# Kernel tuning notes

Hardware: AMD Instinct MI355X
Metric: run time of the kernel (lower is better)

Reference implementation:

```python
import jax, jax.numpy as jnp
import numpy as np

N = 524288   # total graph nodes
V = 64       # number of virtual nodes (clusters)
C = N // V   # nodes per cluster (8192)
D = 256      # in_feats
H = 256      # hidden_feats
EPS = 1e-5


def setup_inputs() -> dict:
    key = jax.random.key(0)
    ks = jax.random.split(key, 8)
    sD = 1.0 / np.sqrt(D)
    sH = 1.0 / np.sqrt(2 * H)
    inp = {
        "x": jax.random.normal(ks[0], (N, D), dtype=jnp.float32),
        "vn_emb": jax.random.normal(ks[1], (V, D), dtype=jnp.float32) * 0.1,
        "wq": jax.random.normal(ks[2], (D, D), dtype=jnp.float32) * sD,
        "wk": jax.random.normal(ks[3], (D, D), dtype=jnp.float32) * sD,
        "v_attn": jax.random.normal(ks[4], (D,), dtype=jnp.float32) * sD,
        "w1": jax.random.normal(ks[5], (D, 2 * H), dtype=jnp.float32) * sD,
        "b1": jnp.zeros((2 * H,), dtype=jnp.float32),
        "g1": jnp.ones((2 * H,), dtype=jnp.float32),
        "beta1": jnp.zeros((2 * H,), dtype=jnp.float32),
        "w2": jax.random.normal(ks[6], (2 * H, H), dtype=jnp.float32) * sH,
        "b2": jnp.zeros((H,), dtype=jnp.float32),
        "g2": jnp.ones((H,), dtype=jnp.float32),
        "beta2": jnp.zeros((H,), dtype=jnp.float32),
        # cluster v owns contiguous node block [v*C, (v+1)*C)
        "vn_index": jnp.arange(N, dtype=jnp.int32).reshape(V, C),
        "vn_indices": jnp.stack(
            [jnp.arange(N, dtype=jnp.int32), (jnp.arange(N, dtype=jnp.int32) // C)],
            axis=1),
    }
    return inp


def _batchnorm(z, g, b):
    # training-mode BN over the virtual-node batch dim
    m = jnp.mean(z, axis=0)
    v = jnp.var(z, axis=0)
    return (z - m) * jax.lax.rsqrt(v + EPS) * g + b


def reference(x, vn_emb, wq, wk, v_attn, w1, b1, g1, beta1,
              w2, b2, g2, beta2, vn_index, vn_indices):
    vx = vn_emb                                   # [V, D]
    # --- update_node_emb (layer 0): broadcast-add VN emb to its nodes ---
    h = x + vx[vn_indices[:, 1]]                  # [N, D]
    # --- update_vn_emb: per-cluster additive attention pooling (vectorized over V) ---
    cluster_h = h[vn_index]                       # [V, C, D]
    q = vx @ wq                                   # [V, D]
    kproj = jnp.einsum('vcd,de->vce', cluster_h, wk)   # [V, C, D]
    scores = jnp.einsum('vce,e->vc', jnp.tanh(kproj + q[:, None, :]), v_attn)
    attn = jax.nn.softmax(scores, axis=-1)        # [V, C]
    pooled = jnp.einsum('vc,vcd->vd', attn, cluster_h) + vx  # [V, D]
    # --- mlp_vns[0]: Linear -> BN -> ReLU -> Linear -> BN -> ReLU ---
    z = jax.nn.relu(_batchnorm(pooled @ w1 + b1, g1, beta1))  # [V, 2H]
    vx_new = jax.nn.relu(_batchnorm(z @ w2 + b2, g2, beta2))  # [V, H]
    return h, vx_new
```

## Files before the change

kernel.cpp:

```cpp
#include <hip/hip_runtime.h>


typedef __bf16 bf16x8 __attribute__((ext_vector_type(8)));
typedef float f32x4 __attribute__((ext_vector_type(4)));
typedef unsigned short us8 __attribute__((ext_vector_type(8)));

__device__ __forceinline__ unsigned short f2bf(float f) {
  unsigned int u = __float_as_uint(f);
  return (unsigned short)((u + 0x7fffu + ((u >> 16) & 1u)) >> 16);
}
__device__ __forceinline__ float tanh_fast(float x) {
  float cx = fminf(fmaxf(x, -15.f), 15.f);
  float e = __expf(2.f * cx);
  return (e - 1.f) * __builtin_amdgcn_rcpf(e + 1.f);
}
__device__ __forceinline__ float wave_sum(float v) {
#pragma unroll
  for (int o = 1; o < 64; o <<= 1) v += __shfl_xor(v, o);
  return v;
}
__device__ __forceinline__ void lgkm_barrier() {
  asm volatile("s_waitcnt lgkmcnt(0)" ::: "memory");
  __builtin_amdgcn_sched_barrier(0);
  __builtin_amdgcn_s_barrier();
  __builtin_amdgcn_sched_barrier(0);
}
__device__ __forceinline__ void gll16(const float* gp, float* lp) {
  __builtin_amdgcn_global_load_lds(
      (const __attribute__((address_space(1))) void*)gp,
      (__attribute__((address_space(3))) void*)lp, 16, 0, 0);
}

__global__ __launch_bounds__(256) void k_prep(
    const float* __restrict__ vn_emb, const float* __restrict__ wq,
    const float* __restrict__ wk, float* __restrict__ qg,
    unsigned short* __restrict__ wkp) {
  int t = threadIdx.x;
  int b = blockIdx.x;
  if (b < 64) {
    float a = 0.f;
#pragma unroll 4
    for (int d = 0; d < 256; ++d) a += vn_emb[(b << 8) + d] * wq[(d << 8) + t];
    qg[(b << 8) + t] = a;
  } else {
    int tid = ((b - 64) << 8) + t;
    int l = tid & 63;
    int ks = (tid >> 6) & 7;
    int ct = tid >> 9;
    int col = (ct << 4) + (l & 15);
    int d0 = (ks << 5) + ((l >> 4) << 3);
    us8 o;
#pragma unroll
    for (int e = 0; e < 8; ++e) o[e] = f2bf(wk[(d0 + e) * 256 + col]);
    *reinterpret_cast<us8*>(wkp + (size_t)tid * 8) = o;
  }
}

__global__ __launch_bounds__(512, 2) void k_main(
    const float* __restrict__ x, const float* __restrict__ vn_emb,
    const float* __restrict__ v_attn, const float* __restrict__ qg,
    const unsigned short* __restrict__ wkp, float* __restrict__ hout,
    float* __restrict__ vecs, float* __restrict__ Zb) {
  __shared__ float stage[2][32 * 256];
  __shared__ unsigned short hs[32 * 256];
  __shared__ float vxs[256], qv[256], va[256];
  __shared__ float spbuf[8][32];

  const int t = threadIdx.x;
  const int blk = blockIdx.x;
  const int cl = blk >> 2;

  if (t < 256) {
    vxs[t] = vn_emb[(cl << 8) + t];
    qv[t] = qg[(cl << 8) + t];
    va[t] = v_attn[t];
  }

  const int l = t & 63, wv = t >> 6;
  const int lr = l & 15, lg = l >> 4;
  const int rg = wv & 1, ctq = wv >> 1;

  bf16x8 wkf[4][8];
#pragma unroll
  for (int c = 0; c < 4; ++c)
#pragma unroll
    for (int ks = 0; ks < 8; ++ks) {
      const int ct = (ctq << 2) + c;
      wkf[c][ks] = __builtin_bit_cast(
          bf16x8, *reinterpret_cast<const us8*>(
                      wkp + ((size_t)((((ct << 3) + ks) << 6) + l)) * 8));
    }

  char* hsb = reinterpret_cast<char*>(hs);
  const size_t growbase = ((size_t)blk << 11) + (wv << 2);
  const int srow0 = wv << 2;

  f32x4 acc = {0.f, 0.f, 0.f, 0.f};
  float zacc = 0.f;

#pragma unroll
  for (int tt = 0; tt < 2; ++tt)
#pragma unroll
    for (int i = 0; i < 4; ++i)
      gll16(x + (((growbase + (tt << 5) + i) << 8) + (l << 2)),
            &stage[tt][(srow0 + i) << 8]);

  __syncthreads();

  const f32x4 vv = *reinterpret_cast<const f32x4*>(&vxs[l << 2]);
  f32x4 hh0, hh1, hh2, hh3;

  for (int tile = 0; tile < 64; ++tile) {
    if (tile == 63) {
      asm volatile("s_waitcnt vmcnt(0)" ::: "memory");
    } else {
      asm volatile("s_waitcnt vmcnt(4)" ::: "memory");
    }
    __builtin_amdgcn_sched_barrier(0);

    const float* sb = &stage[tile & 1][0];
    const size_t hg0 = ((growbase + ((size_t)tile << 5)) << 8) + (l << 2);
#define S1(hhX, i)                                                          \
  {                                                                         \
    f32x4 sv = *reinterpret_cast<const f32x4*>(                             \
        &sb[((srow0 + i) << 8) + (l << 2)]);                                \
    hhX = sv + vv;                                                          \
    *reinterpret_cast<f32x4*>(hout + hg0 + ((size_t)i << 8)) = hhX;         \
    ushort4 o;                                                              \
    o.x = f2bf(hhX[0]);                                                     \
    o.y = f2bf(hhX[1]);                                                     \
    o.z = f2bf(hhX[2]);                                                     \
    o.w = f2bf(hhX[3]);                                                     \
    int row = srow0 + i;                                                    \
    *reinterpret_cast<ushort4*>(                                            \
        hsb + ((row << 9) + ((l << 3) ^ ((row & 7) << 4)))) = o;            \
  }
    S1(hh0, 0) S1(hh1, 1) S1(hh2, 2) S1(hh3, 3)
#undef S1

    __builtin_amdgcn_sched_barrier(0);
    if (tile < 62) {
      const int tt = tile + 2;
#pragma unroll
      for (int i = 0; i < 4; ++i)
        gll16(x + (((growbase + ((size_t)tt << 5) + i) << 8) + (l << 2)),
              &stage[tile & 1][(srow0 + i) << 8]);
    }
    lgkm_barrier();

    bf16x8 bfr[8];
    {
      int row2 = (rg << 4) + lr;
      int sw = (row2 & 7) << 4;
#pragma unroll
      for (int ks = 0; ks < 8; ++ks)
        bfr[ks] = __builtin_bit_cast(
            bf16x8, *reinterpret_cast<const us8*>(
                        hsb + ((row2 << 9) + ((((ks << 6) + (lg << 4))) ^ sw))));
    }
    float sp = 0.f;
#pragma unroll
    for (int c = 0; c < 4; ++c) {
      const int ct = (ctq << 2) + c;
      f32x4 ac0 = {0.f, 0.f, 0.f, 0.f};
#pragma unroll
      for (int ks = 0; ks < 8; ++ks)
        ac0 = __builtin_amdgcn_mfma_f32_16x16x32_bf16(wkf[c][ks], bfr[ks], ac0,
                                                      0, 0, 0);
      const int eo0 = (ct << 4) + (lg << 2);
      const f32x4 qf = *reinterpret_cast<const f32x4*>(&qv[eo0]);
      const f32x4 vf = *reinterpret_cast<const f32x4*>(&va[eo0]);
#pragma unroll
      for (int r = 0; r < 4; ++r) sp += tanh_fast(ac0[r] + qf[r]) * vf[r];
    }
    sp += __shfl_xor(sp, 16);
    sp += __shfl_xor(sp, 32);
    if (lg == 0) spbuf[(ctq << 1) | rg][lr | (rg << 4)] = sp;
    lgkm_barrier();

    float srow = 0.f;
    if (l < 32) {
      int rh = l >> 4;
#pragma unroll
      for (int q = 0; q < 4; ++q) srow += spbuf[(q << 1) | rh][l];
    }
    float w_all = __expf(srow);
    if (wv == 0 && l < 32) zacc += w_all;
    {
      float wn0 = __shfl(w_all, srow0 + 0);
      float wn1 = __shfl(w_all, srow0 + 1);
      float wn2 = __shfl(w_all, srow0 + 2);
      float wn3 = __shfl(w_all, srow0 + 3);
      acc += wn0 * hh0 + wn1 * hh1 + wn2 * hh2 + wn3 * hh3;
    }
  }

  __syncthreads();
  float* sc = reinterpret_cast<float*>(hs);
  *reinterpret_cast<f32x4*>(&sc[(wv << 8) + (l << 2)]) = acc;
  __syncthreads();
  if (t < 256) {
    float s = 0.f;
#pragma unroll
    for (int w8 = 0; w8 < 8; ++w8) s += sc[(w8 << 8) + t];
    vecs[((size_t)blk << 8) + t] = s;
  }
  if (wv == 0) {
    float z = wave_sum(zacc);
    if (l == 0) Zb[blk] = z;
  }
}

__global__ __launch_bounds__(256) void k_combine(
    const float* __restrict__ vecs, const float* __restrict__ Zb,
    const float* __restrict__ vn_emb, float* __restrict__ pooledT) {
  int v = blockIdx.x, t = threadIdx.x;
  float s = 0.f, z = 0.f;
#pragma unroll
  for (int b = 0; b < 4; ++b) {
    s += vecs[(size_t)(((v << 2) + b) << 8) + t];
    z += Zb[(v << 2) + b];
  }
  pooledT[(t << 6) + v] = s / z + vn_emb[(v << 8) + t];
}

__global__ __launch_bounds__(64) void k_mlp1(
    const float* __restrict__ pooledT, const float* __restrict__ w1,
    const float* __restrict__ b1, const float* __restrict__ g1,
    const float* __restrict__ be1, float* __restrict__ z1T) {
  int j = blockIdx.x, v = threadIdx.x;
  float a = 0.f;
#pragma unroll 4
  for (int d = 0; d < 256; ++d) a += pooledT[(d << 6) + v] * w1[(d << 9) + j];
  a += b1[j];
  float mu = wave_sum(a) * (1.f / 64.f);
  float df = a - mu;
  float var = wave_sum(df * df) * (1.f / 64.f);
  float z = df * rsqrtf(var + 1e-5f) * g1[j] + be1[j];
  z1T[(j << 6) + v] = fmaxf(z, 0.f);
}

__global__ __launch_bounds__(64) void k_mlp2(
    const float* __restrict__ z1T, const float* __restrict__ w2,
    const float* __restrict__ b2, const float* __restrict__ g2,
    const float* __restrict__ be2, float* __restrict__ vout) {
  int j = blockIdx.x, v = threadIdx.x;
  float a = 0.f;
#pragma unroll 4
  for (int k = 0; k < 512; ++k) a += z1T[(k << 6) + v] * w2[(k << 8) + j];
  a += b2[j];
  float mu = wave_sum(a) * (1.f / 64.f);
  float df = a - mu;
  float var = wave_sum(df * df) * (1.f / 64.f);
  float z = df * rsqrtf(var + 1e-5f) * g2[j] + be2[j];
  vout[(v << 8) + j] = fmaxf(z, 0.f);
}

extern "C" void kernel_launch(void* const* d_in, const int* in_sizes, int n_in,
                              void* d_out, int out_size, void* d_ws,
                              size_t ws_size, hipStream_t stream) {
  const float* x = (const float*)d_in[0];
  const float* vn_emb = (const float*)d_in[1];
  const float* wq = (const float*)d_in[2];
  const float* wk = (const float*)d_in[3];
  const float* v_attn = (const float*)d_in[4];
  const float* w1 = (const float*)d_in[5];
  const float* b1 = (const float*)d_in[6];
  const float* g1 = (const float*)d_in[7];
  const float* beta1 = (const float*)d_in[8];
  const float* w2 = (const float*)d_in[9];
  const float* b2 = (const float*)d_in[10];
  const float* g2 = (const float*)d_in[11];
  const float* beta2 = (const float*)d_in[12];

  char* wsb = (char*)d_ws;
  float* qg = (float*)(wsb + 0);
  unsigned short* wkp = (unsigned short*)(wsb + 65536);
  float* vecs = (float*)(wsb + 196608);
  float* Zb = (float*)(wsb + 458752);
  float* pooledT = (float*)(wsb + 462848);
  float* z1T = (float*)(wsb + 528384);

  float* hout = (float*)d_out;
  float* vout = hout + (size_t)524288 * 256;

  k_prep<<<96, 256, 0, stream>>>(vn_emb, wq, wk, qg, wkp);
  k_main<<<256, 512, 0, stream>>>(x, vn_emb, v_attn, qg, wkp, hout, vecs, Zb);
  k_combine<<<64, 256, 0, stream>>>(vecs, Zb, vn_emb, pooledT);
  k_mlp1<<<512, 64, 0, stream>>>(pooledT, w1, b1, g1, beta1, z1T);
  k_mlp2<<<256, 64, 0, stream>>>(z1T, w2, b2, g2, beta2, vout);
}
```

Before: 325.8 us.

## Split fused main kernel into streaming h-write pass and separate bf16 pooling pass

Replaces the single fused kernel (256 blocks, which computes h, stages it in LDS and does the MFMA attention pooling) with two kernels when the workspace is large enough. A simple streaming kernel writes h and a bf16 copy of h to workspace. A second 1024-block kernel reads the bf16 copy and computes the attention scores and weighted pooling. The goal is more parallelism and simpler bandwidth-bound streaming, at the cost of an extra 256MB write and read of the bf16 intermediate. Pooling also now accumulates from bf16-rounded h rather than fp32.

```diff
diff --git a/kernel.cpp b/kernel.cpp
--- a/kernel.cpp
+++ b/kernel.cpp
@@ -8,6 +8,9 @@
 __device__ __forceinline__ unsigned short f2bf(float f) {
   unsigned int u = __float_as_uint(f);
   return (unsigned short)((u + 0x7fffu + ((u >> 16) & 1u)) >> 16);
+}
+__device__ __forceinline__ float bf2f(unsigned short s) {
+  return __uint_as_float(((unsigned int)s) << 16);
 }
 __device__ __forceinline__ float tanh_fast(float x) {
   float cx = fminf(fmaxf(x, -15.f), 15.f);
@@ -56,6 +59,122 @@
   }
 }
 
+__global__ __launch_bounds__(256) void k_stream(
+    const float* __restrict__ x, const float* __restrict__ vn_emb,
+    float* __restrict__ hout, ushort4* __restrict__ hbf4) {
+  const int t = threadIdx.x, blk = blockIdx.x;
+  const int cl = blk >> 6;
+  const size_t base = ((size_t)blk << 13);
+  const f32x4 vv = *reinterpret_cast<const f32x4*>(
+      &vn_emb[(cl << 8) + ((t & 63) << 2)]);
+  const f32x4* xv = reinterpret_cast<const f32x4*>(x);
+  f32x4* hv = reinterpret_cast<f32x4*>(hout);
+#pragma unroll 8
+  for (int i = 0; i < 32; ++i) {
+    const size_t id = base + (i << 8) + t;
+    f32x4 h = xv[id] + vv;
+    hv[id] = h;
+    ushort4 o;
+    o.x = f2bf(h[0]);
+    o.y = f2bf(h[1]);
+    o.z = f2bf(h[2]);
+    o.w = f2bf(h[3]);
+    hbf4[id] = o;
+  }
+}
+
+__global__ __launch_bounds__(256, 3) void k_pool(
+    const ushort4* __restrict__ hbf4, const float* __restrict__ v_attn,
+    const float* __restrict__ qg, const unsigned short* __restrict__ wkp,
+    float* __restrict__ vecs, float* __restrict__ Zb) {
+  __shared__ unsigned short hs[4][16 * 256];
+  __shared__ float qv[256], va[256];
+  __shared__ float zr[4];
+
+  const int t = threadIdx.x;
+  const int blk = blockIdx.x;
+  const int cl = blk >> 4;
+
+  qv[t] = qg[(cl << 8) + t];
+  va[t] = v_attn[t];
+  __syncthreads();
+
+  const int l = t & 63, wv = t >> 6;
+  const int lr = l & 15, lg = l >> 4;
+
+  char* myhs = reinterpret_cast<char*>(hs[wv]);
+  f32x4 acc = {0.f, 0.f, 0.f, 0.f};
+  float zacc = 0.f;
+
+  const size_t wrow0 = ((size_t)blk << 9) + ((size_t)wv << 7);
+
+  for (int chunk = 0; chunk < 8; ++chunk) {
+    const size_t row0 = wrow0 + ((size_t)chunk << 4);
+
+#pragma unroll
+    for (int i = 0; i < 16; ++i) {
+      ushort4 hv4 = hbf4[((row0 + i) << 6) + l];
+      *reinterpret_cast<ushort4*>(
+          myhs + ((i << 9) + ((l << 3) ^ ((i & 7) << 4)))) = hv4;
+    }
+    asm volatile("s_waitcnt lgkmcnt(0)" ::: "memory");
+    __builtin_amdgcn_sched_barrier(0);
+
+    bf16x8 bfr[8];
+    {
+      const int sw = (lr & 7) << 4;
+#pragma unroll
+      for (int ks = 0; ks < 8; ++ks)
+        bfr[ks] = __builtin_bit_cast(
+            bf16x8, *reinterpret_cast<const us8*>(
+                        myhs + ((lr << 9) + ((((ks << 6) + (lg << 4))) ^ sw))));
+    }
+
+    float sp = 0.f;
+#pragma unroll 4
+    for (int ct = 0; ct < 16; ++ct) {
+      f32x4 ac0 = {0.f, 0.f, 0.f, 0.f};
+#pragma unroll
+      for (int ks = 0; ks < 8; ++ks) {
+        bf16x8 af = __builtin_bit_cast(
+            bf16x8, *reinterpret_cast<const us8*>(
+                        wkp + ((size_t)((((ct << 3) + ks) << 6) + l)) * 8));
+        ac0 = __builtin_amdgcn_mfma_f32_16x16x32_bf16(af, bfr[ks], ac0, 0, 0, 0);
+      }
+      const int eo0 = (ct << 4) + (lg << 2);
+      const f32x4 qf = *reinterpret_cast<const f32x4*>(&qv[eo0]);
+      const f32x4 vf = *reinterpret_cast<const f32x4*>(&va[eo0]);
+#pragma unroll
+      for (int r = 0; r < 4; ++r) sp += tanh_fast(ac0[r] + qf[r]) * vf[r];
+    }
+    sp += __shfl_xor(sp, 16);
+    sp += __shfl_xor(sp, 32);
+    float w = __expf(sp);
+    zacc += w;
+
+#pragma unroll
+    for (int n = 0; n < 16; ++n) {
+      float wn = __shfl(w, n);
+      ushort4 hv4 = *reinterpret_cast<const ushort4*>(
+          myhs + ((n << 9) + ((l << 3) ^ ((n & 7) << 4))));
+      acc[0] += wn * bf2f(hv4.x);
+      acc[1] += wn * bf2f(hv4.y);
+      acc[2] += wn * bf2f(hv4.z);
+      acc[3] += wn * bf2f(hv4.w);
+    }
+  }
+
+  __syncthreads();
+  float* sc = reinterpret_cast<float*>(hs);
+  *reinterpret_cast<f32x4*>(&sc[(wv << 8) + (l << 2)]) = acc;
+  float zsum = wave_sum(zacc) * 0.25f;
+  if (l == 0) zr[wv] = zsum;
+  __syncthreads();
+  vecs[((size_t)blk << 8) + t] =
+      sc[t] + sc[256 + t] + sc[512 + t] + sc[768 + t];
+  if (t == 0) Zb[blk] = zr[0] + zr[1] + zr[2] + zr[3];
+}
+
 __global__ __launch_bounds__(512, 2) void k_main(
     const float* __restrict__ x, const float* __restrict__ vn_emb,
     const float* __restrict__ v_attn, const float* __restrict__ qg,
@@ -213,13 +332,12 @@
 
 __global__ __launch_bounds__(256) void k_combine(
     const float* __restrict__ vecs, const float* __restrict__ Zb,
-    const float* __restrict__ vn_emb, float* __restrict__ pooledT) {
+    const float* __restrict__ vn_emb, float* __restrict__ pooledT, int nb) {
   int v = blockIdx.x, t = threadIdx.x;
   float s = 0.f, z = 0.f;
-#pragma unroll
-  for (int b = 0; b < 4; ++b) {
-    s += vecs[(size_t)(((v << 2) + b) << 8) + t];
-    z += Zb[(v << 2) + b];
+  for (int b = 0; b < nb; ++b) {
+    s += vecs[((size_t)(v * nb + b) << 8) + t];
+    z += Zb[v * nb + b];
   }
   pooledT[(t << 6) + v] = s / z + vn_emb[(v << 8) + t];
 }
@@ -277,16 +395,27 @@
   float* qg = (float*)(wsb + 0);
   unsigned short* wkp = (unsigned short*)(wsb + 65536);
   float* vecs = (float*)(wsb + 196608);
-  float* Zb = (float*)(wsb + 458752);
-  float* pooledT = (float*)(wsb + 462848);
-  float* z1T = (float*)(wsb + 528384);
+  float* Zb = (float*)(wsb + 1245184);
+  float* pooledT = (float*)(wsb + 1253376);
+  float* z1T = (float*)(wsb + 1318912);
+  ushort4* hbf4 = (ushort4*)(wsb + 2097152);
+
+  const size_t need_big = 2097152 + (size_t)524288 * 256 * 2;
+  const bool big = ws_size >= need_big;
 
   float* hout = (float*)d_out;
   float* vout = hout + (size_t)524288 * 256;
 
   k_prep<<<96, 256, 0, stream>>>(vn_emb, wq, wk, qg, wkp);
-  k_main<<<256, 512, 0, stream>>>(x, vn_emb, v_attn, qg, wkp, hout, vecs, Zb);
-  k_combine<<<64, 256, 0, stream>>>(vecs, Zb, vn_emb, pooledT);
+  if (big) {
+    k_stream<<<4096, 256, 0, stream>>>(x, vn_emb, hout, hbf4);
+    k_pool<<<1024, 256, 0, stream>>>(hbf4, v_attn, qg, wkp, vecs, Zb);
+    k_combine<<<64, 256, 0, stream>>>(vecs, Zb, vn_emb, pooledT, 16);
+  } else {
+    k_main<<<256, 512, 0, stream>>>(x, vn_emb, v_attn, qg, wkp, hout, vecs,
+                                    Zb);
+    k_combine<<<64, 256, 0, stream>>>(vecs, Zb, vn_emb, pooledT, 4);
+  }
   k_mlp1<<<512, 64, 0, stream>>>(pooledT, w1, b1, g1, beta1, z1T);
   k_mlp2<<<256, 64, 0, stream>>>(z1T, w2, b2, g2, beta2, vout);
 }
```

Result: slower. 649.1 us (+99.2%).

## Double wave count in main kernel to 16 waves per 1024-thread block

Applied to the files above, without the earlier changes.

Reworks the main attention-pooling kernel to run 16 waves per block instead of 8. Each wave now owns one 16-column output tile of the key projection and streams two rows per tile instead of four. Each wave also holds a quarter of the previous weight-fragment registers and hoists the q/v_attn loads out of the loop. The aim is more waves in flight per CU to hide memory latency on this streaming kernel. The cost is more barrier participants, a larger score-reduction buffer and fewer outstanding loads per wave.

```diff
diff --git a/kernel.cpp b/kernel.cpp
--- a/kernel.cpp
+++ b/kernel.cpp
@@ -56,7 +56,7 @@
   }
 }
 
-__global__ __launch_bounds__(512, 2) void k_main(
+__global__ __launch_bounds__(1024) void k_main16(
     const float* __restrict__ x, const float* __restrict__ vn_emb,
     const float* __restrict__ v_attn, const float* __restrict__ qg,
     const unsigned short* __restrict__ wkp, float* __restrict__ hout,
@@ -64,7 +64,7 @@
   __shared__ float stage[2][32 * 256];
   __shared__ unsigned short hs[32 * 256];
   __shared__ float vxs[256], qv[256], va[256];
-  __shared__ float spbuf[8][32];
+  __shared__ float spbuf[16][32];
 
   const int t = threadIdx.x;
   const int blk = blockIdx.x;
@@ -78,22 +78,18 @@
 
   const int l = t & 63, wv = t >> 6;
   const int lr = l & 15, lg = l >> 4;
-  const int rg = wv & 1, ctq = wv >> 1;
-
-  bf16x8 wkf[4][8];
-#pragma unroll
-  for (int c = 0; c < 4; ++c)
-#pragma unroll
-    for (int ks = 0; ks < 8; ++ks) {
-      const int ct = (ctq << 2) + c;
-      wkf[c][ks] = __builtin_bit_cast(
-          bf16x8, *reinterpret_cast<const us8*>(
-                      wkp + ((size_t)((((ct << 3) + ks) << 6) + l)) * 8));
-    }
+  const int ct = wv;
+  const int srow0 = wv << 1;
+
+  bf16x8 wkf[8];
+#pragma unroll
+  for (int ks = 0; ks < 8; ++ks)
+    wkf[ks] = __builtin_bit_cast(
+        bf16x8, *reinterpret_cast<const us8*>(
+                    wkp + ((size_t)((((ct << 3) + ks) << 6) + l)) * 8));
 
   char* hsb = reinterpret_cast<char*>(hs);
-  const size_t growbase = ((size_t)blk << 11) + (wv << 2);
-  const int srow0 = wv << 2;
+  const size_t growbase = ((size_t)blk << 11) + srow0;
 
   f32x4 acc = {0.f, 0.f, 0.f, 0.f};
   float zacc = 0.f;
@@ -101,20 +97,23 @@
 #pragma unroll
   for (int tt = 0; tt < 2; ++tt)
 #pragma unroll
-    for (int i = 0; i < 4; ++i)
+    for (int i = 0; i < 2; ++i)
       gll16(x + (((growbase + (tt << 5) + i) << 8) + (l << 2)),
             &stage[tt][(srow0 + i) << 8]);
 
   __syncthreads();
 
   const f32x4 vv = *reinterpret_cast<const f32x4*>(&vxs[l << 2]);
-  f32x4 hh0, hh1, hh2, hh3;
+  const int eo0 = (ct << 4) + (lg << 2);
+  const f32x4 qf = *reinterpret_cast<const f32x4*>(&qv[eo0]);
+  const f32x4 vf = *reinterpret_cast<const f32x4*>(&va[eo0]);
+  f32x4 hh0, hh1;
 
   for (int tile = 0; tile < 64; ++tile) {
     if (tile == 63) {
       asm volatile("s_waitcnt vmcnt(0)" ::: "memory");
     } else {
-      asm volatile("s_waitcnt vmcnt(4)" ::: "memory");
+      asm volatile("s_waitcnt vmcnt(2)" ::: "memory");
     }
     __builtin_amdgcn_sched_barrier(0);
 
@@ -135,63 +134,57 @@
     *reinterpret_cast<ushort4*>(                                            \
         hsb + ((row << 9) + ((l << 3) ^ ((row & 7) << 4)))) = o;            \
   }
-    S1(hh0, 0) S1(hh1, 1) S1(hh2, 2) S1(hh3, 3)
+    S1(hh0, 0) S1(hh1, 1)
 #undef S1
 
     __builtin_amdgcn_sched_barrier(0);
     if (tile < 62) {
       const int tt = tile + 2;
 #pragma unroll
-      for (int i = 0; i < 4; ++i)
+      for (int i = 0; i < 2; ++i)
         gll16(x + (((growbase + ((size_t)tt << 5) + i) << 8) + (l << 2)),
               &stage[tile & 1][(srow0 + i) << 8]);
     }
     lgkm_barrier();
 
-    bf16x8 bfr[8];
-    {
-      int row2 = (rg << 4) + lr;
-      int sw = (row2 & 7) << 4;
+#pragma unroll
+    for (int rg = 0; rg < 2; ++rg) {
+      bf16x8 bfr[8];
+      {
+        int row2 = (rg << 4) + lr;
+        int sw = (row2 & 7) << 4;
+#pragma unroll
+        for (int ks = 0; ks < 8; ++ks)
+          bfr[ks] = __builtin_bit_cast(
+              bf16x8,
+              *reinterpret_cast<const us8*>(
+                  hsb + ((row2 << 9) + ((((ks << 6) + (lg << 4))) ^ sw))));
+      }
+      f32x4 ac0 = {0.f, 0.f, 0.f, 0.f};
 #pragma unroll
       for (int ks = 0; ks < 8; ++ks)
-        bfr[ks] = __builtin_bit_cast(
-            bf16x8, *reinterpret_cast<const us8*>(
-                        hsb + ((row2 << 9) + ((((ks << 6) + (lg << 4))) ^ sw))));
-    }
-    float sp = 0.f;
-#pragma unroll
-    for (int c = 0; c < 4; ++c) {
-      const int ct = (ctq << 2) + c;
-      f32x4 ac0 = {0.f, 0.f, 0.f, 0.f};
-#pragma unroll
-      for (int ks = 0; ks < 8; ++ks)
-        ac0 = __builtin_amdgcn_mfma_f32_16x16x32_bf16(wkf[c][ks], bfr[ks], ac0,
-                                                      0, 0, 0);
-      const int eo0 = (ct << 4) + (lg << 2);
-      const f32x4 qf = *reinterpret_cast<const f32x4*>(&qv[eo0]);
-      const f32x4 vf = *reinterpret_cast<const f32x4*>(&va[eo0]);
+        ac0 = __builtin_amdgcn_mfma_f32_16x16x32_bf16(wkf[ks], bfr[ks], ac0, 0,
+                                                      0, 0);
+      float sp = 0.f;
 #pragma unroll
       for (int r = 0; r < 4; ++r) sp += tanh_fast(ac0[r] + qf[r]) * vf[r];
-    }
-    sp += __shfl_xor(sp, 16);
-    sp += __shfl_xor(sp, 32);
-    if (lg == 0) spbuf[(ctq << 1) | rg][lr | (rg << 4)] = sp;
+      sp += __shfl_xor(sp, 16);
+      sp += __shfl_xor(sp, 32);
+      if (lg == 0) spbuf[ct][(rg << 4) + lr] = sp;
+    }
     lgkm_barrier();
 
     float srow = 0.f;
     if (l < 32) {
-      int rh = l >> 4;
-#pragma unroll
-      for (int q = 0; q < 4; ++q) srow += spbuf[(q << 1) | rh][l];
+#pragma unroll
+      for (int q = 0; q < 16; ++q) srow += spbuf[q][l];
     }
     float w_all = __expf(srow);
     if (wv == 0 && l < 32) zacc += w_all;
     {
       float wn0 = __shfl(w_all, srow0 + 0);
       float wn1 = __shfl(w_all, srow0 + 1);
-      float wn2 = __shfl(w_all, srow0 + 2);
-      float wn3 = __shfl(w_all, srow0 + 3);
-      acc += wn0 * hh0 + wn1 * hh1 + wn2 * hh2 + wn3 * hh3;
+      acc += wn0 * hh0 + wn1 * hh1;
     }
   }
 
@@ -202,7 +195,7 @@
   if (t < 256) {
     float s = 0.f;
 #pragma unroll
-    for (int w8 = 0; w8 < 8; ++w8) s += sc[(w8 << 8) + t];
+    for (int w16 = 0; w16 < 16; ++w16) s += sc[(w16 << 8) + t];
     vecs[((size_t)blk << 8) + t] = s;
   }
   if (wv == 0) {
@@ -285,7 +278,8 @@
   float* vout = hout + (size_t)524288 * 256;
 
   k_prep<<<96, 256, 0, stream>>>(vn_emb, wq, wk, qg, wkp);
-  k_main<<<256, 512, 0, stream>>>(x, vn_emb, v_attn, qg, wkp, hout, vecs, Zb);
+  k_main16<<<256, 1024, 0, stream>>>(x, vn_emb, v_attn, qg, wkp, hout, vecs,
+                                     Zb);
   k_combine<<<64, 256, 0, stream>>>(vecs, Zb, vn_emb, pooledT);
   k_mlp1<<<512, 64, 0, stream>>>(pooledT, w1, b1, g1, beta1, z1T);
   k_mlp2<<<256, 64, 0, stream>>>(z1T, w2, b2, g2, beta2, vout);
```

Measured after the change: 324.4 us (median of 2 runs). About the same (-0.4%).
